# Performance work log

Measured on AMD Instinct MI355X. Metric: run time of the kernel, lower is better.

## Reference

```python
import jax, jax.numpy as jnp
import numpy as np
from jax import lax


def setup_inputs() -> dict:
    key = jax.random.key(0)
    k1, k2 = jax.random.split(key)
    B, C = 128, 256
    z_f = jax.random.normal(k1, (B, C, 7, 7), dtype=jnp.float32)
    x_f = jax.random.normal(k2, (B, C, 31, 31), dtype=jnp.float32)
    return {"z_f": z_f, "x_f": x_f}


def xcorr_depthwise(search, kernel):
    # search: [B, C, Hx, Wx], kernel: [B, C, Hz, Wz]
    B, C, Hx, Wx = search.shape
    _, _, Hz, Wz = kernel.shape
    s = search.reshape(1, B * C, Hx, Wx)          # [1, B*C, Hx, Wx]
    k = kernel.reshape(B * C, 1, Hz, Wz)          # [B*C, 1, Hz, Wz]
    out = lax.conv_general_dilated(
        s, k,
        window_strides=(1, 1),
        padding='VALID',
        dimension_numbers=('NCHW', 'OIHW', 'NCHW'),
        feature_group_count=B * C,
    )                                             # [1, B*C, Ho, Wo]
    Ho, Wo = Hx - Hz + 1, Wx - Wz + 1
    return out.reshape(B, C, Ho, Wo)


def reference(z_f, x_f):
    # DepthwiseRPN.forward: xcorr_depthwise(search=x_f, kernel=z_f)
    return xcorr_depthwise(x_f, z_f)
```

## Files before the change

### kernel.cpp

```cpp
#include <hip/hip_runtime.h>


#define PPB 5
#define WX 31
#define XPLANE 961
#define RS 41
#define LPLANE 1280
#define NCH (PPB * 10)
#define ZPLANE 49
#define ZFLOATS (PPB * ZPLANE)
#define OPLANE 625
#define WO 25

typedef __attribute__((address_space(1))) const void gaddr_t;
typedef __attribute__((address_space(3))) void laddr_t;

__global__ __launch_bounds__(128, 2) void dwxcorr_kernel(
    const float* __restrict__ z, const float* __restrict__ x,
    float* __restrict__ out, int nplanes) {
  __shared__ float xs[PPB * LPLANE];
  __shared__ float zs[256];

  const int tid = threadIdx.x;
  const int wbase = tid & ~63;
  const int p0 = blockIdx.x * PPB;
  const int pmax = min(PPB, nplanes - p0);
  const long XTOT = (long)nplanes * XPLANE;
  const long ZTOT = (long)nplanes * ZPLANE;
  const long xoff = (long)p0 * XPLANE;
  const long zoff = (long)p0 * ZPLANE;

  int offx[10];
#pragma unroll
  for (int i = 0; i < 10; ++i) {
    int s = i * 128 + tid;
    int r = s / RS;
    int col = s - r * RS;
    r = (r > 30) ? 30 : r;
    col = (col > 30) ? 30 : col;
    offx[i] = r * WX + col;
  }

#pragma unroll
  for (int c = 0; c < NCH; ++c) {
    const int pp = c / 10;
    const int i = c - pp * 10;
    long gi = xoff + pp * XPLANE + offx[i];
    if (gi >= XTOT) gi = XTOT - 1;
    __builtin_amdgcn_global_load_lds((gaddr_t*)(x + gi),
                                     (laddr_t*)&xs[c * 128 + wbase], 4, 0, 0);
  }
#pragma unroll
  for (int c = 0; c < 2; ++c) {
    long gi = zoff + c * 128 + tid;
    if (gi >= ZTOT) gi = ZTOT - 1;
    __builtin_amdgcn_global_load_lds((gaddr_t*)(z + gi),
                                     (laddr_t*)&zs[c * 128 + wbase], 4, 0, 0);
  }
  __syncthreads();

  const int cpp = tid / 25;
  if (tid >= PPB * 25 || cpp >= pmax) return;
  const int t25 = tid - cpp * 25;
  const int ty = t25 / 5;
  const int tx = t25 - ty * 5;
  const int tx5 = tx * 5;

  float zr[ZPLANE];
#pragma unroll
  for (int j = 0; j < ZPLANE; ++j) zr[j] = zs[cpp * ZPLANE + j];

  float acc[5][5];
#pragma unroll
  for (int r = 0; r < 5; ++r)
#pragma unroll
    for (int j = 0; j < 5; ++j) acc[r][j] = 0.0f;

  const float* pb = &xs[cpp * LPLANE + (ty * 5) * RS + tx5];

#pragma unroll
  for (int iy = 0; iy < 11; ++iy) {
    float xr[11];
#pragma unroll
    for (int k = 0; k < 11; ++k) xr[k] = pb[iy * RS + k];
    const int ky_lo = (iy - 4 < 0) ? 0 : iy - 4;
    const int ky_hi = (iy < 6) ? iy : 6;
#pragma unroll
    for (int ky = 0; ky < 7; ++ky) {
      if (ky < ky_lo || ky > ky_hi) continue;
      const int orow = iy - ky;
#pragma unroll
      for (int kx = 0; kx < 7; ++kx) {
        const float zv = zr[ky * 7 + kx];
#pragma unroll
        for (int j = 0; j < 5; ++j)
          acc[orow][j] = fmaf(xr[kx + j], zv, acc[orow][j]);
      }
    }
  }

  float* ob = out + (long)(p0 + cpp) * OPLANE + (ty * 5) * WO + tx5;
#pragma unroll
  for (int r = 0; r < 5; ++r)
#pragma unroll
    for (int j = 0; j < 5; ++j) ob[r * WO + j] = acc[r][j];
}

extern "C" void kernel_launch(void* const* d_in, const int* in_sizes, int n_in,
                              void* d_out, int out_size, void* d_ws, size_t ws_size,
                              hipStream_t stream) {
  const float* z = (const float*)d_in[0];
  const float* x = (const float*)d_in[1];
  float* out = (float*)d_out;

  const int nplanes = in_sizes[0] / ZPLANE;
  const int blocks = (nplanes + PPB - 1) / PPB;

  hipLaunchKernelGGL(dwxcorr_kernel, dim3(blocks), dim3(128), 0, stream,
                     z, x, out, nplanes);
}
```

Before: 53.51 us.

## Load x planes contiguously into LDS with native stride and raise occupancy

Replaces the padded 41-stride LDS layout (requiring per-thread offset computation and clamped gathers) with a flat contiguous copy of 5 planes using the native 31-element row stride, cutting the LDS chunks from 50 to 38 and shrinking shared memory. A fast path skips bounds clamping for full interior blocks. Launch bounds are raised to 4 blocks per CU to allow more occupancy. The odd 31 stride may introduce LDS bank conflicts on the register-load phase, and the higher occupancy target may constrain register allocation for the 49 z values and 25 accumulators.

After: 54.32 us. No clear change (+1.5%).

```diff
diff --git a/kernel.cpp b/kernel.cpp
--- a/kernel.cpp
+++ b/kernel.cpp
@@ -4,58 +4,61 @@
 #define PPB 5
 #define WX 31
 #define XPLANE 961
-#define RS 41
-#define LPLANE 1280
-#define NCH (PPB * 10)
+#define TDW (PPB * XPLANE)
+#define XCH 38
+#define XREG (XCH * 128)
 #define ZPLANE 49
-#define ZFLOATS (PPB * ZPLANE)
+#define ZDW (PPB * ZPLANE)
+#define ZREG 256
 #define OPLANE 625
 #define WO 25
 
 typedef __attribute__((address_space(1))) const void gaddr_t;
 typedef __attribute__((address_space(3))) void laddr_t;
 
-__global__ __launch_bounds__(128, 2) void dwxcorr_kernel(
+__global__ __launch_bounds__(128, 4) void dwxcorr_kernel(
     const float* __restrict__ z, const float* __restrict__ x,
     float* __restrict__ out, int nplanes) {
-  __shared__ float xs[PPB * LPLANE];
-  __shared__ float zs[256];
+  __shared__ float xs[XREG];
+  __shared__ float zs[ZREG];
 
   const int tid = threadIdx.x;
   const int wbase = tid & ~63;
   const int p0 = blockIdx.x * PPB;
   const int pmax = min(PPB, nplanes - p0);
-  const long XTOT = (long)nplanes * XPLANE;
-  const long ZTOT = (long)nplanes * ZPLANE;
   const long xoff = (long)p0 * XPLANE;
   const long zoff = (long)p0 * ZPLANE;
 
-  int offx[10];
+  if (pmax == PPB && (long)(blockIdx.x + 1) * TDW + 59 <= (long)nplanes * XPLANE) {
 #pragma unroll
-  for (int i = 0; i < 10; ++i) {
-    int s = i * 128 + tid;
-    int r = s / RS;
-    int col = s - r * RS;
-    r = (r > 30) ? 30 : r;
-    col = (col > 30) ? 30 : col;
-    offx[i] = r * WX + col;
-  }
-
+    for (int c = 0; c < XCH; ++c)
+      __builtin_amdgcn_global_load_lds((gaddr_t*)(x + xoff + c * 128 + tid),
+                                       (laddr_t*)&xs[c * 128 + wbase], 4, 0, 0);
 #pragma unroll
-  for (int c = 0; c < NCH; ++c) {
-    const int pp = c / 10;
-    const int i = c - pp * 10;
-    long gi = xoff + pp * XPLANE + offx[i];
-    if (gi >= XTOT) gi = XTOT - 1;
-    __builtin_amdgcn_global_load_lds((gaddr_t*)(x + gi),
-                                     (laddr_t*)&xs[c * 128 + wbase], 4, 0, 0);
-  }
+    for (int c = 0; c < 2; ++c) {
+      long gz = zoff + c * 128 + tid;
+      long zmax = (long)nplanes * ZPLANE - 1;
+      if (gz > zmax) gz = zmax;
+      __builtin_amdgcn_global_load_lds((gaddr_t*)(z + gz),
+                                       (laddr_t*)&zs[c * 128 + wbase], 4, 0, 0);
+    }
+  } else {
+    const long xmax = (long)nplanes * XPLANE - 1;
+    const long zmax = (long)nplanes * ZPLANE - 1;
 #pragma unroll
-  for (int c = 0; c < 2; ++c) {
-    long gi = zoff + c * 128 + tid;
-    if (gi >= ZTOT) gi = ZTOT - 1;
-    __builtin_amdgcn_global_load_lds((gaddr_t*)(z + gi),
-                                     (laddr_t*)&zs[c * 128 + wbase], 4, 0, 0);
+    for (int c = 0; c < XCH; ++c) {
+      long gi = xoff + c * 128 + tid;
+      if (gi > xmax) gi = xmax;
+      __builtin_amdgcn_global_load_lds((gaddr_t*)(x + gi),
+                                       (laddr_t*)&xs[c * 128 + wbase], 4, 0, 0);
+    }
+#pragma unroll
+    for (int c = 0; c < 2; ++c) {
+      long gz = zoff + c * 128 + tid;
+      if (gz > zmax) gz = zmax;
+      __builtin_amdgcn_global_load_lds((gaddr_t*)(z + gz),
+                                       (laddr_t*)&zs[c * 128 + wbase], 4, 0, 0);
+    }
   }
   __syncthreads();
 
@@ -76,13 +79,13 @@
 #pragma unroll
     for (int j = 0; j < 5; ++j) acc[r][j] = 0.0f;
 
-  const float* pb = &xs[cpp * LPLANE + (ty * 5) * RS + tx5];
+  const float* pb = &xs[cpp * XPLANE + (ty * 5) * WX + tx5];
 
 #pragma unroll
   for (int iy = 0; iy < 11; ++iy) {
     float xr[11];
 #pragma unroll
-    for (int k = 0; k < 11; ++k) xr[k] = pb[iy * RS + k];
+    for (int k = 0; k < 11; ++k) xr[k] = pb[iy * WX + k];
     const int ky_lo = (iy - 4 < 0) ? 0 : iy - 4;
     const int ky_hi = (iy < 6) ? iy : 6;
 #pragma unroll
```
